# Kernel tuning notes

Hardware: AMD Instinct MI355X
Metric: run time of the kernel (lower is better)

## Reference

```python
import jax, jax.numpy as jnp
import numpy as np

C_IN, C_OUT, K, H, W = 16, 16, 3, 1024, 1024
PAD = 1  # 'same' padding for 3x3 stride-1


def setup_inputs() -> dict:
    key = jax.random.key(0)
    kx, kw, kb = jax.random.split(key, 3)
    x = jax.random.normal(kx, (1, C_IN, H, W), dtype=jnp.float32)
    weight = jax.random.normal(kw, (C_OUT, C_IN, K, K), dtype=jnp.float32) * 0.05
    bias = jax.random.normal(kb, (C_OUT,), dtype=jnp.float32) * 0.05
    return {"x": x, "weight": weight, "bias": bias}


def reference(x, weight, bias):
    # Original module: im2col (unfold) + matmul + reshape + bias add.
    # Mathematically identical to a dense 2D convolution (cross-correlation),
    # expressed here as the fused implicit-GEMM conv primitive.
    out = jax.lax.conv_general_dilated(
        x, weight,
        window_strides=(1, 1),
        padding=((PAD, PAD), (PAD, PAD)),
        dimension_numbers=("NCHW", "OIHW", "NCHW"),
    )  # [1, C_OUT, H, W]
    # out_unf.view(*output_shape) drops the batch dim (batch must be 1)
    return out[0] + bias[:, None, None]
```

## Files before the change

kernel.cpp:

```cpp
#include <hip/hip_runtime.h>


#define HH 1024
#define WW 1024
#define CIN 16
#define COUT 16
#define TW 64
#define TH 16
#define LROWS (TH + 2)
#define LCOLS (TW + 2)
#define PIX 16
#define NPIX (LROWS * LCOLS)

typedef short v8s __attribute__((ext_vector_type(8)));
typedef float v4f __attribute__((ext_vector_type(4)));
typedef unsigned int u32;

__device__ __forceinline__ unsigned short f32_bf16(float f) {
    union { float f; u32 u; } v;
    v.f = f;
    u32 u = v.u;
    u += 0x7fffu + ((u >> 16) & 1u);
    return (unsigned short)(u >> 16);
}

__device__ __forceinline__ int swz(int c) { return c ^ ((c >> 3) & 7); }

__global__ __launch_bounds__(256, 3)
void conv3x3_fused(const float* __restrict__ x,
                   const float* __restrict__ wgt,
                   const float* __restrict__ bias,
                   float* __restrict__ out) {
    __shared__ __align__(16) unsigned short sm[NPIX * PIX];
    __shared__ __align__(16) unsigned short wsm[20 * 16 * 8];

    const int tid = threadIdx.x;
    const int lane = tid & 63;
    const int wave = tid >> 6;
    const int h0 = blockIdx.y * TH;
    const int w0 = blockIdx.x * TW;

    if (tid < 32) ((uint4*)(wsm + 18 * 16 * 8))[tid] = make_uint4(0u, 0u, 0u, 0u);
    #pragma unroll
    for (int s = 0; s < 9; ++s) {
        const int e = s * 256 + tid;
        const int m = e / 144;
        const int rem = e - m * 144;
        const int c = rem / 9;
        const int r9 = rem - c * 9;
        const int t = r9 * 2 + (c >> 3);
        wsm[(t * 16 + m) * 8 + (c & 7)] = f32_bf16(wgt[e]);
    }

    auto stage_body = [&](int b) {
        const int r = b >> 4;
        const int j = b & 15;
        const int gh = h0 - 1 + r;
        const int pbase = r * LCOLS + 1 + 4 * j;
        float4 f4[CIN];
        if ((unsigned)gh < (unsigned)HH) {
            const float4* src = (const float4*)(x + (size_t)gh * WW + w0) + j;
            #pragma unroll
            for (int c = 0; c < CIN; ++c)
                f4[c] = src[(size_t)c * (HH * WW / 4)];
        } else {
            #pragma unroll
            for (int c = 0; c < CIN; ++c)
                f4[c] = make_float4(0.f, 0.f, 0.f, 0.f);
        }
        #pragma unroll
        for (int k = 0; k < 4; ++k) {
            u32 pk[8];
            #pragma unroll
            for (int i = 0; i < 8; ++i) {
                const float lo = ((const float*)&f4[2 * i])[k];
                const float hi = ((const float*)&f4[2 * i + 1])[k];
                pk[i] = (u32)f32_bf16(lo) | ((u32)f32_bf16(hi) << 16);
            }
            #pragma unroll
            for (int half = 0; half < 2; ++half) {
                const int cc = 2 * pbase + 2 * k + half;
                *(uint4*)(sm + swz(cc) * 8) = *(uint4*)&pk[half * 4];
            }
        }
    };
    auto stage_halo = [&](int h) {
        const int r = h >> 1;
        const int side = h & 1;
        const int gh = h0 - 1 + r;
        const int gw = side ? (w0 + 64) : (w0 - 1);
        const int p = r * LCOLS + (side ? 65 : 0);
        float f[CIN];
        if ((unsigned)gh < (unsigned)HH && (unsigned)gw < (unsigned)WW) {
            const float* src = x + (size_t)gh * WW + gw;
            #pragma unroll
            for (int c = 0; c < CIN; ++c) f[c] = src[(size_t)c * (HH * WW)];
        } else {
            #pragma unroll
            for (int c = 0; c < CIN; ++c) f[c] = 0.f;
        }
        u32 pk[8];
        #pragma unroll
        for (int i = 0; i < 8; ++i)
            pk[i] = (u32)f32_bf16(f[2 * i]) | ((u32)f32_bf16(f[2 * i + 1]) << 16);
        #pragma unroll
        for (int half = 0; half < 2; ++half) {
            const int cc = 2 * p + half;
            *(uint4*)(sm + swz(cc) * 8) = *(uint4*)&pk[half * 4];
        }
    };

    stage_body(tid);
    if (tid < 32) stage_body(256 + tid);
    else if (tid < 68) stage_halo(tid - 32);

    const int m = lane & 15;
    const int q = lane >> 4;
    const int colbase = wave * 16 + m;

    int Kofs[5];
    #pragma unroll
    for (int g5 = 0; g5 < 5; ++g5) {
        int t = 4 * g5 + q;
        int tt = t > 17 ? 17 : t;
        int khkw = tt >> 1;
        int kh = khkw / 3;
        int kw = khkw - 3 * kh;
        int half = tt & 1;
        Kofs[g5] = (kh * LCOLS + colbase + kw) * 2 + half;
    }
    float bl[4];
    #pragma unroll
    for (int i = 0; i < 4; ++i) bl[i] = bias[q * 4 + i];

    __syncthreads();

    v8s a[5];
    #pragma unroll
    for (int g5 = 0; g5 < 5; ++g5) {
        const int t = 4 * g5 + q;
        a[g5] = *(const v8s*)(wsm + (t * 16 + m) * 8);
    }

    #pragma unroll 4
    for (int r = 0; r < TH; ++r) {
        v4f acc = {0.f, 0.f, 0.f, 0.f};
        #pragma unroll
        for (int g5 = 0; g5 < 5; ++g5) {
            int c = r * (LCOLS * 2) + Kofs[g5];
            v8s b = *(const v8s*)(sm + swz(c) * 8);
            acc = __builtin_amdgcn_mfma_f32_16x16x32_bf16(a[g5], b, acc, 0, 0, 0);
        }
        float* op = out + (size_t)(h0 + r) * WW + (w0 + colbase);
        #pragma unroll
        for (int i = 0; i < 4; ++i)
            op[(size_t)(q * 4 + i) * (HH * WW)] = acc[i] + bl[i];
    }
}

extern "C" void kernel_launch(void* const* d_in, const int* in_sizes, int n_in,
                              void* d_out, int out_size, void* d_ws, size_t ws_size,
                              hipStream_t stream) {
    const float* x = (const float*)d_in[0];
    const float* w = (const float*)d_in[1];
    const float* b = (const float*)d_in[2];
    float* out = (float*)d_out;
    dim3 grid(WW / TW, HH / TH);
    conv3x3_fused<<<grid, dim3(256), 0, stream>>>(x, w, b, out);
}
```

Measured before the change: 128.9 us.

## Process two row tiles per block with register-prefetched next tile

Each block now handles two vertical 16-row tiles. The second tile's input is loaded into registers before the first tile is computed, then written to LDS after a barrier. This hides global load latency behind the MFMA work and amortizes the weight conversion across both tiles. It also replaces the manual bf16 rounding with the packed v_cvt_pk_bf16_f32 instruction. The cost is much higher register pressure from the prefetch buffers, so launch bounds drop to 2 blocks per CU and the grid is halved, which may reduce occupancy and parallelism.

New measurement: 127.8 us. No clear change (-0.9%).

```diff
diff --git a/kernel.cpp b/kernel.cpp
--- a/kernel.cpp
+++ b/kernel.cpp
@@ -7,6 +7,7 @@
 #define COUT 16
 #define TW 64
 #define TH 16
+#define NT 2
 #define LROWS (TH + 2)
 #define LCOLS (TW + 2)
 #define PIX 16
@@ -24,9 +25,15 @@
     return (unsigned short)(u >> 16);
 }
 
+__device__ __forceinline__ u32 cvt_pk_bf16(float lo, float hi) {
+    u32 r;
+    asm("v_cvt_pk_bf16_f32 %0, %1, %2" : "=v"(r) : "v"(lo), "v"(hi));
+    return r;
+}
+
 __device__ __forceinline__ int swz(int c) { return c ^ ((c >> 3) & 7); }
 
-__global__ __launch_bounds__(256, 3)
+__global__ __launch_bounds__(256, 2)
 void conv3x3_fused(const float* __restrict__ x,
                    const float* __restrict__ wgt,
                    const float* __restrict__ bias,
@@ -37,7 +44,7 @@
     const int tid = threadIdx.x;
     const int lane = tid & 63;
     const int wave = tid >> 6;
-    const int h0 = blockIdx.y * TH;
+    const int h0a = blockIdx.y * (TH * NT);
     const int w0 = blockIdx.x * TW;
 
     if (tid < 32) ((uint4*)(wsm + 18 * 16 * 8))[tid] = make_uint4(0u, 0u, 0u, 0u);
@@ -52,12 +59,10 @@
         wsm[(t * 16 + m) * 8 + (c & 7)] = f32_bf16(wgt[e]);
     }
 
-    auto stage_body = [&](int b) {
+    auto load_body = [&](int b, int h0, float4* f4) {
         const int r = b >> 4;
         const int j = b & 15;
         const int gh = h0 - 1 + r;
-        const int pbase = r * LCOLS + 1 + 4 * j;
-        float4 f4[CIN];
         if ((unsigned)gh < (unsigned)HH) {
             const float4* src = (const float4*)(x + (size_t)gh * WW + w0) + j;
             #pragma unroll
@@ -68,6 +73,11 @@
             for (int c = 0; c < CIN; ++c)
                 f4[c] = make_float4(0.f, 0.f, 0.f, 0.f);
         }
+    };
+    auto write_body = [&](int b, const float4* f4) {
+        const int r = b >> 4;
+        const int j = b & 15;
+        const int pbase = r * LCOLS + 1 + 4 * j;
         #pragma unroll
         for (int k = 0; k < 4; ++k) {
             u32 pk[8];
@@ -75,7 +85,7 @@
             for (int i = 0; i < 8; ++i) {
                 const float lo = ((const float*)&f4[2 * i])[k];
                 const float hi = ((const float*)&f4[2 * i + 1])[k];
-                pk[i] = (u32)f32_bf16(lo) | ((u32)f32_bf16(hi) << 16);
+                pk[i] = cvt_pk_bf16(lo, hi);
             }
             #pragma unroll
             for (int half = 0; half < 2; ++half) {
@@ -84,13 +94,11 @@
             }
         }
     };
-    auto stage_halo = [&](int h) {
+    auto load_halo = [&](int h, int h0, float* f) {
         const int r = h >> 1;
         const int side = h & 1;
         const int gh = h0 - 1 + r;
-        const int gw = side ? (w0 + 64) : (w0 - 1);
-        const int p = r * LCOLS + (side ? 65 : 0);
-        float f[CIN];
+        const int gw = side ? (w0 + TW) : (w0 - 1);
         if ((unsigned)gh < (unsigned)HH && (unsigned)gw < (unsigned)WW) {
             const float* src = x + (size_t)gh * WW + gw;
             #pragma unroll
@@ -99,10 +107,15 @@
             #pragma unroll
             for (int c = 0; c < CIN; ++c) f[c] = 0.f;
         }
+    };
+    auto write_halo = [&](int h, const float* f) {
+        const int r = h >> 1;
+        const int side = h & 1;
+        const int p = r * LCOLS + (side ? 65 : 0);
         u32 pk[8];
         #pragma unroll
         for (int i = 0; i < 8; ++i)
-            pk[i] = (u32)f32_bf16(f[2 * i]) | ((u32)f32_bf16(f[2 * i + 1]) << 16);
+            pk[i] = cvt_pk_bf16(f[2 * i], f[2 * i + 1]);
         #pragma unroll
         for (int half = 0; half < 2; ++half) {
             const int cc = 2 * p + half;
@@ -110,9 +123,17 @@
         }
     };
 
-    stage_body(tid);
-    if (tid < 32) stage_body(256 + tid);
-    else if (tid < 68) stage_halo(tid - 32);
+    {
+        float4 f1[16];
+        float4 f2[16];
+        float fh[16];
+        load_body(tid, h0a, f1);
+        if (tid < 32) load_body(256 + tid, h0a, f2);
+        else if (tid < 68) load_halo(tid - 32, h0a, fh);
+        write_body(tid, f1);
+        if (tid < 32) write_body(256 + tid, f2);
+        else if (tid < 68) write_halo(tid - 32, fh);
+    }
 
     const int m = lane & 15;
     const int q = lane >> 4;
@@ -135,6 +156,13 @@
 
     __syncthreads();
 
+    float4 p1[16];
+    float4 p2[16];
+    float ph[16];
+    load_body(tid, h0a + TH, p1);
+    if (tid < 32) load_body(256 + tid, h0a + TH, p2);
+    else if (tid < 68) load_halo(tid - 32, h0a + TH, ph);
+
     v8s a[5];
     #pragma unroll
     for (int g5 = 0; g5 < 5; ++g5) {
@@ -142,20 +170,34 @@
         a[g5] = *(const v8s*)(wsm + (t * 16 + m) * 8);
     }
 
-    #pragma unroll 4
-    for (int r = 0; r < TH; ++r) {
-        v4f acc = {0.f, 0.f, 0.f, 0.f};
-        #pragma unroll
-        for (int g5 = 0; g5 < 5; ++g5) {
-            int c = r * (LCOLS * 2) + Kofs[g5];
-            v8s b = *(const v8s*)(sm + swz(c) * 8);
-            acc = __builtin_amdgcn_mfma_f32_16x16x32_bf16(a[g5], b, acc, 0, 0, 0);
-        }
-        float* op = out + (size_t)(h0 + r) * WW + (w0 + colbase);
-        #pragma unroll
-        for (int i = 0; i < 4; ++i)
-            op[(size_t)(q * 4 + i) * (HH * WW)] = acc[i] + bl[i];
-    }
+    auto compute_tile = [&](int h0) {
+        #pragma unroll 4
+        for (int r = 0; r < TH; ++r) {
+            v4f acc = {0.f, 0.f, 0.f, 0.f};
+            #pragma unroll
+            for (int g5 = 0; g5 < 5; ++g5) {
+                const int c = r * (LCOLS * 2) + Kofs[g5];
+                v8s b = *(const v8s*)(sm + swz(c) * 8);
+                acc = __builtin_amdgcn_mfma_f32_16x16x32_bf16(a[g5], b, acc, 0, 0, 0);
+            }
+            float* op = out + (size_t)(h0 + r) * WW + (w0 + colbase);
+            #pragma unroll
+            for (int i = 0; i < 4; ++i)
+                op[(size_t)(q * 4 + i) * (HH * WW)] = acc[i] + bl[i];
+        }
+    };
+
+    compute_tile(h0a);
+
+    __syncthreads();
+
+    write_body(tid, p1);
+    if (tid < 32) write_body(256 + tid, p2);
+    else if (tid < 68) write_halo(tid - 32, ph);
+
+    __syncthreads();
+
+    compute_tile(h0a + TH);
 }
 
 extern "C" void kernel_launch(void* const* d_in, const int* in_sizes, int n_in,
@@ -165,6 +207,6 @@
     const float* w = (const float*)d_in[1];
     const float* b = (const float*)d_in[2];
     float* out = (float*)d_out;
-    dim3 grid(WW / TW, HH / TH);
+    dim3 grid(WW / TW, HH / (TH * NT));
     conv3x3_fused<<<grid, dim3(256), 0, stream>>>(x, w, b, out);
 }
```

## Process four row tiles per block with double-buffered LDS and register prefetch

Applied to the files above, without the earlier changes.

Each block now handles four vertically stacked 16-row tiles using 512 threads. The next tile's input is loaded into registers while the current tile is computed, then written to the other half of a double-buffered LDS array. This amortizes the weight staging, reduces the number of blocks, and hides global load latency behind MFMA work. Float-to-bf16 packing now uses the hardware v_cvt_pk_bf16_f32 instruction. The costs are fewer blocks in flight (256 total, launch bounds of 1), higher register pressure from two prefetch buffers, and a tail where the last tile's compute cannot overlap any load.

Measured after the change: 126.3 us. 1.02x faster.

```diff
diff --git a/kernel.cpp b/kernel.cpp
--- a/kernel.cpp
+++ b/kernel.cpp
@@ -7,10 +7,12 @@
 #define COUT 16
 #define TW 64
 #define TH 16
+#define NT 4
 #define LROWS (TH + 2)
 #define LCOLS (TW + 2)
 #define PIX 16
 #define NPIX (LROWS * LCOLS)
+#define SMHALF (NPIX * PIX)
 
 typedef short v8s __attribute__((ext_vector_type(8)));
 typedef float v4f __attribute__((ext_vector_type(4)));
@@ -24,99 +26,117 @@
     return (unsigned short)(u >> 16);
 }
 
+__device__ __forceinline__ u32 cvt_pk_bf16(float lo, float hi) {
+    u32 r;
+    asm("v_cvt_pk_bf16_f32 %0, %1, %2" : "=v"(r) : "v"(lo), "v"(hi));
+    return r;
+}
+
 __device__ __forceinline__ int swz(int c) { return c ^ ((c >> 3) & 7); }
 
-__global__ __launch_bounds__(256, 3)
+__global__ __launch_bounds__(512, 1)
 void conv3x3_fused(const float* __restrict__ x,
                    const float* __restrict__ wgt,
                    const float* __restrict__ bias,
                    float* __restrict__ out) {
-    __shared__ __align__(16) unsigned short sm[NPIX * PIX];
+    __shared__ __align__(16) unsigned short sm[2 * SMHALF];
     __shared__ __align__(16) unsigned short wsm[20 * 16 * 8];
 
     const int tid = threadIdx.x;
     const int lane = tid & 63;
     const int wave = tid >> 6;
-    const int h0 = blockIdx.y * TH;
+    const int h0blk = blockIdx.y * (TH * NT);
     const int w0 = blockIdx.x * TW;
 
     if (tid < 32) ((uint4*)(wsm + 18 * 16 * 8))[tid] = make_uint4(0u, 0u, 0u, 0u);
     #pragma unroll
-    for (int s = 0; s < 9; ++s) {
-        const int e = s * 256 + tid;
-        const int m = e / 144;
-        const int rem = e - m * 144;
-        const int c = rem / 9;
-        const int r9 = rem - c * 9;
-        const int t = r9 * 2 + (c >> 3);
-        wsm[(t * 16 + m) * 8 + (c & 7)] = f32_bf16(wgt[e]);
+    for (int s = 0; s < 5; ++s) {
+        const int e = s * 512 + tid;
+        if (e < 2304) {
+            const int m = e / 144;
+            const int rem = e - m * 144;
+            const int c = rem / 9;
+            const int r9 = rem - c * 9;
+            const int t = r9 * 2 + (c >> 3);
+            wsm[(t * 16 + m) * 8 + (c & 7)] = f32_bf16(wgt[e]);
+        }
     }
 
-    auto stage_body = [&](int b) {
-        const int r = b >> 4;
-        const int j = b & 15;
-        const int gh = h0 - 1 + r;
-        const int pbase = r * LCOLS + 1 + 4 * j;
-        float4 f4[CIN];
-        if ((unsigned)gh < (unsigned)HH) {
-            const float4* src = (const float4*)(x + (size_t)gh * WW + w0) + j;
-            #pragma unroll
-            for (int c = 0; c < CIN; ++c)
-                f4[c] = src[(size_t)c * (HH * WW / 4)];
-        } else {
-            #pragma unroll
-            for (int c = 0; c < CIN; ++c)
-                f4[c] = make_float4(0.f, 0.f, 0.f, 0.f);
-        }
-        #pragma unroll
-        for (int k = 0; k < 4; ++k) {
+    auto load_tile = [&](int t, float4* f4, float* fh) {
+        const int h0 = h0blk + t * TH;
+        if (tid < 288) {
+            const int r = tid >> 4;
+            const int j = tid & 15;
+            const int gh = h0 - 1 + r;
+            if ((unsigned)gh < (unsigned)HH) {
+                const float4* src = (const float4*)(x + (size_t)gh * WW + w0) + j;
+                #pragma unroll
+                for (int c = 0; c < CIN; ++c)
+                    f4[c] = src[(size_t)c * (HH * WW / 4)];
+            } else {
+                #pragma unroll
+                for (int c = 0; c < CIN; ++c)
+                    f4[c] = make_float4(0.f, 0.f, 0.f, 0.f);
+            }
+        } else if (tid < 324) {
+            const int h = tid - 288;
+            const int r = h >> 1;
+            const int side = h & 1;
+            const int gh = h0 - 1 + r;
+            const int gw = side ? (w0 + TW) : (w0 - 1);
+            if ((unsigned)gh < (unsigned)HH && (unsigned)gw < (unsigned)WW) {
+                const float* src = x + (size_t)gh * WW + gw;
+                #pragma unroll
+                for (int c = 0; c < CIN; ++c) fh[c] = src[(size_t)c * (HH * WW)];
+            } else {
+                #pragma unroll
+                for (int c = 0; c < CIN; ++c) fh[c] = 0.f;
+            }
+        }
+    };
+    auto write_tile = [&](int t, const float4* f4, const float* fh) {
+        unsigned short* smb = sm + (t & 1) * SMHALF;
+        if (tid < 288) {
+            const int r = tid >> 4;
+            const int j = tid & 15;
+            const int pbase = r * LCOLS + 1 + 4 * j;
+            #pragma unroll
+            for (int k = 0; k < 4; ++k) {
+                u32 pk[8];
+                #pragma unroll
+                for (int i = 0; i < 8; ++i) {
+                    const float lo = ((const float*)&f4[2 * i])[k];
+                    const float hi = ((const float*)&f4[2 * i + 1])[k];
+                    pk[i] = cvt_pk_bf16(lo, hi);
+                }
+                #pragma unroll
+                for (int half = 0; half < 2; ++half) {
+                    const int cc = 2 * pbase + 2 * k + half;
+                    *(uint4*)(smb + swz(cc) * 8) = *(uint4*)&pk[half * 4];
+                }
+            }
+        } else if (tid < 324) {
+            const int h = tid - 288;
+            const int r = h >> 1;
+            const int side = h & 1;
+            const int p = r * LCOLS + (side ? 65 : 0);
             u32 pk[8];
             #pragma unroll
-            for (int i = 0; i < 8; ++i) {
-                const float lo = ((const float*)&f4[2 * i])[k];
-                const float hi = ((const float*)&f4[2 * i + 1])[k];
-                pk[i] = (u32)f32_bf16(lo) | ((u32)f32_bf16(hi) << 16);
-            }
+            for (int i = 0; i < 8; ++i)
+                pk[i] = cvt_pk_bf16(fh[2 * i], fh[2 * i + 1]);
             #pragma unroll
             for (int half = 0; half < 2; ++half) {
-                const int cc = 2 * pbase + 2 * k + half;
-                *(uint4*)(sm + swz(cc) * 8) = *(uint4*)&pk[half * 4];
+                const int cc = 2 * p + half;
+                *(uint4*)(smb + swz(cc) * 8) = *(uint4*)&pk[half * 4];
             }
         }
     };
-    auto stage_halo = [&](int h) {
-        const int r = h >> 1;
-        const int side = h & 1;
-        const int gh = h0 - 1 + r;
-        const int gw = side ? (w0 + 64) : (w0 - 1);
-        const int p = r * LCOLS + (side ? 65 : 0);
-        float f[CIN];
-        if ((unsigned)gh < (unsigned)HH && (unsigned)gw < (unsigned)WW) {
-            const float* src = x + (size_t)gh * WW + gw;
-            #pragma unroll
-            for (int c = 0; c < CIN; ++c) f[c] = src[(size_t)c * (HH * WW)];
-        } else {
-            #pragma unroll
-            for (int c = 0; c < CIN; ++c) f[c] = 0.f;
-        }
-        u32 pk[8];
-        #pragma unroll
-        for (int i = 0; i < 8; ++i)
-            pk[i] = (u32)f32_bf16(f[2 * i]) | ((u32)f32_bf16(f[2 * i + 1]) << 16);
-        #pragma unroll
-        for (int half = 0; half < 2; ++half) {
-            const int cc = 2 * p + half;
-            *(uint4*)(sm + swz(cc) * 8) = *(uint4*)&pk[half * 4];
-        }
-    };
-
-    stage_body(tid);
-    if (tid < 32) stage_body(256 + tid);
-    else if (tid < 68) stage_halo(tid - 32);
 
     const int m = lane & 15;
     const int q = lane >> 4;
-    const int colbase = wave * 16 + m;
+    const int wc = wave & 3;
+    const int wq = wave >> 2;
+    const int colbase = wc * 16 + m;
 
     int Kofs[5];
     #pragma unroll
@@ -133,6 +153,10 @@
     #pragma unroll
     for (int i = 0; i < 4; ++i) bl[i] = bias[q * 4 + i];
 
+    float4 fA[CIN]; float hA[CIN];
+    float4 fB[CIN]; float hB[CIN];
+    load_tile(0, fA, hA);
+    write_tile(0, fA, hA);
     __syncthreads();
 
     v8s a[5];
@@ -142,20 +166,42 @@
         a[g5] = *(const v8s*)(wsm + (t * 16 + m) * 8);
     }
 
-    #pragma unroll 4
-    for (int r = 0; r < TH; ++r) {
-        v4f acc = {0.f, 0.f, 0.f, 0.f};
-        #pragma unroll
-        for (int g5 = 0; g5 < 5; ++g5) {
-            int c = r * (LCOLS * 2) + Kofs[g5];
-            v8s b = *(const v8s*)(sm + swz(c) * 8);
-            acc = __builtin_amdgcn_mfma_f32_16x16x32_bf16(a[g5], b, acc, 0, 0, 0);
-        }
-        float* op = out + (size_t)(h0 + r) * WW + (w0 + colbase);
-        #pragma unroll
-        for (int i = 0; i < 4; ++i)
-            op[(size_t)(q * 4 + i) * (HH * WW)] = acc[i] + bl[i];
-    }
+    auto compute_tile = [&](int t) {
+        const unsigned short* smb = sm + (t & 1) * SMHALF;
+        const int h0 = h0blk + t * TH;
+        #pragma unroll 4
+        for (int rr = 0; rr < 8; ++rr) {
+            const int r = wq * 8 + rr;
+            v4f acc = {0.f, 0.f, 0.f, 0.f};
+            #pragma unroll
+            for (int g5 = 0; g5 < 5; ++g5) {
+                const int c = r * (LCOLS * 2) + Kofs[g5];
+                v8s b = *(const v8s*)(smb + swz(c) * 8);
+                acc = __builtin_amdgcn_mfma_f32_16x16x32_bf16(a[g5], b, acc, 0, 0, 0);
+            }
+            float* op = out + (size_t)(h0 + r) * WW + (w0 + colbase);
+            #pragma unroll
+            for (int i = 0; i < 4; ++i)
+                op[(size_t)(q * 4 + i) * (HH * WW)] = acc[i] + bl[i];
+        }
+    };
+
+    load_tile(1, fB, hB);
+    compute_tile(0);
+    write_tile(1, fB, hB);
+    __syncthreads();
+
+    load_tile(2, fA, hA);
+    compute_tile(1);
+    write_tile(2, fA, hA);
+    __syncthreads();
+
+    load_tile(3, fB, hB);
+    compute_tile(2);
+    write_tile(3, fB, hB);
+    __syncthreads();
+
+    compute_tile(3);
 }
 
 extern "C" void kernel_launch(void* const* d_in, const int* in_sizes, int n_in,
@@ -165,6 +211,6 @@
     const float* w = (const float*)d_in[1];
     const float* b = (const float*)d_in[2];
     float* out = (float*)d_out;
-    dim3 grid(WW / TW, HH / TH);
-    conv3x3_fused<<<grid, dim3(256), 0, stream>>>(x, w, b, out);
-}
+    dim3 grid(WW / TW, HH / (TH * NT));
+    conv3x3_fused<<<grid, dim3(512), 0, stream>>>(x, w, b, out);
+}
```

## Restructure conv into single-wave blocks with register-prefetched double tiles

Applied to the files above, without the earlier changes.

Replaces the 256-thread block that staged a 66x18 halo tile with 64-thread single-wave blocks. Each block handles a 16-wide by 32-tall output strip as two 16x16 tiles, prefetching the second tile's input into registers while the first is computed. Weights are converted straight into MFMA operand registers rather than going through shared memory, and the software bf16 rounding is replaced with the hardware v_cvt_pk_bf16_f32 instruction. Dropping block barriers and shared weight staging is meant to cut latency, at the cost of more halo re-reads (18x18 per 16x16 tile), narrower float2 global loads, and heavier register use.

After: 162.3 us. +25.9%, slower.

```diff
diff --git a/kernel.cpp b/kernel.cpp
--- a/kernel.cpp
+++ b/kernel.cpp
@@ -4,119 +4,56 @@
 #define HH 1024
 #define WW 1024
 #define CIN 16
-#define COUT 16
-#define TW 64
-#define TH 16
-#define LROWS (TH + 2)
-#define LCOLS (TW + 2)
-#define PIX 16
-#define NPIX (LROWS * LCOLS)
+#define HWP (HH * WW)
+#define LPX 392
 
 typedef short v8s __attribute__((ext_vector_type(8)));
 typedef float v4f __attribute__((ext_vector_type(4)));
 typedef unsigned int u32;
 
-__device__ __forceinline__ unsigned short f32_bf16(float f) {
-    union { float f; u32 u; } v;
-    v.f = f;
-    u32 u = v.u;
-    u += 0x7fffu + ((u >> 16) & 1u);
-    return (unsigned short)(u >> 16);
+__device__ __forceinline__ u32 cvt_pk_bf16(float lo, float hi) {
+    u32 r;
+    asm("v_cvt_pk_bf16_f32 %0, %1, %2" : "=v"(r) : "v"(lo), "v"(hi));
+    return r;
 }
 
 __device__ __forceinline__ int swz(int c) { return c ^ ((c >> 3) & 7); }
 
-__global__ __launch_bounds__(256, 3)
-void conv3x3_fused(const float* __restrict__ x,
-                   const float* __restrict__ wgt,
-                   const float* __restrict__ bias,
-                   float* __restrict__ out) {
-    __shared__ __align__(16) unsigned short sm[NPIX * PIX];
-    __shared__ __align__(16) unsigned short wsm[20 * 16 * 8];
+__global__ __launch_bounds__(64, 2)
+void conv3x3_wave(const float* __restrict__ x,
+                  const float* __restrict__ wgt,
+                  const float* __restrict__ bias,
+                  float* __restrict__ out) {
+    __shared__ __align__(16) unsigned short sm[LPX * 16];
 
-    const int tid = threadIdx.x;
-    const int lane = tid & 63;
-    const int wave = tid >> 6;
-    const int h0 = blockIdx.y * TH;
-    const int w0 = blockIdx.x * TW;
+    const int lane = threadIdx.x;
+    const int m = lane & 15;
+    const int q = lane >> 4;
+    const int w0 = blockIdx.x * 16;
+    const int h0b = blockIdx.y * 32;
 
-    if (tid < 32) ((uint4*)(wsm + 18 * 16 * 8))[tid] = make_uint4(0u, 0u, 0u, 0u);
+    v8s a[5];
     #pragma unroll
-    for (int s = 0; s < 9; ++s) {
-        const int e = s * 256 + tid;
-        const int m = e / 144;
-        const int rem = e - m * 144;
-        const int c = rem / 9;
-        const int r9 = rem - c * 9;
-        const int t = r9 * 2 + (c >> 3);
-        wsm[(t * 16 + m) * 8 + (c & 7)] = f32_bf16(wgt[e]);
+    for (int g5 = 0; g5 < 5; ++g5) {
+        const int t = 4 * g5 + q;
+        union { u32 u[4]; v8s v; } wv;
+        if (t < 18) {
+            const int base = m * 144 + (t & 1) * 72 + (t >> 1);
+            #pragma unroll
+            for (int jj = 0; jj < 4; ++jj) {
+                const float lo = wgt[base + 18 * jj];
+                const float hi = wgt[base + 18 * jj + 9];
+                wv.u[jj] = cvt_pk_bf16(lo, hi);
+            }
+        } else {
+            wv.u[0] = wv.u[1] = wv.u[2] = wv.u[3] = 0u;
+        }
+        a[g5] = wv.v;
     }
 
-    auto stage_body = [&](int b) {
-        const int r = b >> 4;
-        const int j = b & 15;
-        const int gh = h0 - 1 + r;
-        const int pbase = r * LCOLS + 1 + 4 * j;
-        float4 f4[CIN];
-        if ((unsigned)gh < (unsigned)HH) {
-            const float4* src = (const float4*)(x + (size_t)gh * WW + w0) + j;
-            #pragma unroll
-            for (int c = 0; c < CIN; ++c)
-                f4[c] = src[(size_t)c * (HH * WW / 4)];
-        } else {
-            #pragma unroll
-            for (int c = 0; c < CIN; ++c)
-                f4[c] = make_float4(0.f, 0.f, 0.f, 0.f);
-        }
-        #pragma unroll
-        for (int k = 0; k < 4; ++k) {
-            u32 pk[8];
-            #pragma unroll
-            for (int i = 0; i < 8; ++i) {
-                const float lo = ((const float*)&f4[2 * i])[k];
-                const float hi = ((const float*)&f4[2 * i + 1])[k];
-                pk[i] = (u32)f32_bf16(lo) | ((u32)f32_bf16(hi) << 16);
-            }
-            #pragma unroll
-            for (int half = 0; half < 2; ++half) {
-                const int cc = 2 * pbase + 2 * k + half;
-                *(uint4*)(sm + swz(cc) * 8) = *(uint4*)&pk[half * 4];
-            }
-        }
-    };
-    auto stage_halo = [&](int h) {
-        const int r = h >> 1;
-        const int side = h & 1;
-        const int gh = h0 - 1 + r;
-        const int gw = side ? (w0 + 64) : (w0 - 1);
-        const int p = r * LCOLS + (side ? 65 : 0);
-        float f[CIN];
-        if ((unsigned)gh < (unsigned)HH && (unsigned)gw < (unsigned)WW) {
-            const float* src = x + (size_t)gh * WW + gw;
-            #pragma unroll
-            for (int c = 0; c < CIN; ++c) f[c] = src[(size_t)c * (HH * WW)];
-        } else {
-            #pragma unroll
-            for (int c = 0; c < CIN; ++c) f[c] = 0.f;
-        }
-        u32 pk[8];
-        #pragma unroll
-        for (int i = 0; i < 8; ++i)
-            pk[i] = (u32)f32_bf16(f[2 * i]) | ((u32)f32_bf16(f[2 * i + 1]) << 16);
-        #pragma unroll
-        for (int half = 0; half < 2; ++half) {
-            const int cc = 2 * p + half;
-            *(uint4*)(sm + swz(cc) * 8) = *(uint4*)&pk[half * 4];
-        }
-    };
-
-    stage_body(tid);
-    if (tid < 32) stage_body(256 + tid);
-    else if (tid < 68) stage_halo(tid - 32);
-
-    const int m = lane & 15;
-    const int q = lane >> 4;
-    const int colbase = wave * 16 + m;
+    float bl[4];
+    #pragma unroll
+    for (int i = 0; i < 4; ++i) bl[i] = bias[q * 4 + i];
 
     int Kofs[5];
     #pragma unroll
@@ -126,36 +63,88 @@
         int khkw = tt >> 1;
         int kh = khkw / 3;
         int kw = khkw - 3 * kh;
-        int half = tt & 1;
-        Kofs[g5] = (kh * LCOLS + colbase + kw) * 2 + half;
-    }
-    float bl[4];
-    #pragma unroll
-    for (int i = 0; i < 4; ++i) bl[i] = bias[q * 4 + i];
-
-    __syncthreads();
-
-    v8s a[5];
-    #pragma unroll
-    for (int g5 = 0; g5 < 5; ++g5) {
-        const int t = 4 * g5 + q;
-        a[g5] = *(const v8s*)(wsm + (t * 16 + m) * 8);
+        Kofs[g5] = (kh * 18 + m + kw) * 2 + (tt & 1);
     }
 
-    #pragma unroll 4
-    for (int r = 0; r < TH; ++r) {
-        v4f acc = {0.f, 0.f, 0.f, 0.f};
+    const bool intW = (w0 != 0) && (w0 != WW - 16);
+
+    float2 f[48];
+
+    auto load_tile = [&](int h0) {
+        const bool interior = intW && (h0 != 0) && (h0 != HH - 16);
         #pragma unroll
-        for (int g5 = 0; g5 < 5; ++g5) {
-            int c = r * (LCOLS * 2) + Kofs[g5];
-            v8s b = *(const v8s*)(sm + swz(c) * 8);
-            acc = __builtin_amdgcn_mfma_f32_16x16x32_bf16(a[g5], b, acc, 0, 0, 0);
+        for (int it = 0; it < 3; ++it) {
+            const int T0 = lane + 64 * it;
+            const int T = T0 < 162 ? T0 : 161;
+            const int r = T / 9;
+            const int c = 2 * (T - 9 * r);
+            const int gh = h0 - 1 + r;
+            const int gw = w0 - 1 + c;
+            float2* dst = f + it * 16;
+            if (interior) {
+                const float* p = x + (size_t)gh * WW + gw;
+                #pragma unroll
+                for (int ch = 0; ch < CIN; ++ch)
+                    dst[ch] = *(const float2*)(p + (size_t)ch * HWP);
+            } else {
+                const bool okh = (unsigned)gh < (unsigned)HH;
+                const bool ok0 = okh && (unsigned)gw < (unsigned)WW;
+                const bool ok1 = okh && (unsigned)(gw + 1) < (unsigned)WW;
+                const size_t b0 = (size_t)(okh ? gh : 0) * WW;
+                #pragma unroll
+                for (int ch = 0; ch < CIN; ++ch) {
+                    const float* p = x + (size_t)ch * HWP + b0;
+                    dst[ch].x = ok0 ? p[gw] : 0.f;
+                    dst[ch].y = ok1 ? p[gw + 1] : 0.f;
+                }
+            }
         }
-        float* op = out + (size_t)(h0 + r) * WW + (w0 + colbase);
+    };
+
+    auto write_tile = [&]() {
         #pragma unroll
-        for (int i = 0; i < 4; ++i)
-            op[(size_t)(q * 4 + i) * (HH * WW)] = acc[i] + bl[i];
-    }
+        for (int it = 0; it < 3; ++it) {
+            const int T0 = lane + 64 * it;
+            const bool valid = T0 < 162;
+            const int sl = lane >= 34 ? lane - 34 : 0;
+            const int cb = valid ? 4 * T0 : (648 + 4 * sl);
+            const float2* s = f + it * 16;
+            u32 pk[8], pk2[8];
+            #pragma unroll
+            for (int i = 0; i < 8; ++i) {
+                pk[i]  = cvt_pk_bf16(s[2 * i].x, s[2 * i + 1].x);
+                pk2[i] = cvt_pk_bf16(s[2 * i].y, s[2 * i + 1].y);
+            }
+            *(uint4*)(sm + swz(cb + 0) * 8) = *(uint4*)&pk[0];
+            *(uint4*)(sm + swz(cb + 1) * 8) = *(uint4*)&pk[4];
+            *(uint4*)(sm + swz(cb + 2) * 8) = *(uint4*)&pk2[0];
+            *(uint4*)(sm + swz(cb + 3) * 8) = *(uint4*)&pk2[4];
+        }
+    };
+
+    auto compute_tile = [&](int h0) {
+        #pragma unroll 4
+        for (int r = 0; r < 16; ++r) {
+            v4f acc = {0.f, 0.f, 0.f, 0.f};
+            #pragma unroll
+            for (int g5 = 0; g5 < 5; ++g5) {
+                const int ck = r * 36 + Kofs[g5];
+                v8s b = *(const v8s*)(sm + swz(ck) * 8);
+                acc = __builtin_amdgcn_mfma_f32_16x16x32_bf16(a[g5], b, acc, 0, 0, 0);
+            }
+            float* op = out + (size_t)(h0 + r) * WW + (w0 + m);
+            #pragma unroll
+            for (int i = 0; i < 4; ++i)
+                op[(size_t)(q * 4 + i) * HWP] = acc[i] + bl[i];
+        }
+    };
+
+    load_tile(h0b);
+    write_tile();
+    load_tile(h0b + 16);
+    compute_tile(h0b);
+    write_tile();
+    compute_tile(h0b + 16);
 }
 
 extern "C" void kernel_launch(void* const* d_in, const int* in_sizes, int n_in,
@@ -165,6 +154,6 @@
     const float* w = (const float*)d_in[1];
     const float* b = (const float*)d_in[2];
     float* out = (float*)d_out;
-    dim3 grid(WW / TW, HH / TH);
-    conv3x3_fused<<<grid, dim3(256), 0, stream>>>(x, w, b, out);
+    dim3 grid(WW / 16, HH / 32);
+    conv3x3_wave<<<grid, dim3(64), 0, stream>>>(x, w, b, out);
 }
```
